# Optimization experiments

Measured on AMD Instinct MI355X. Metric: run time of the kernel, lower is better.

Reference implementation:

```python
import jax, jax.numpy as jnp
import numpy as np


def _rotate_half(x):
    x1, x2 = jnp.split(x, 2, axis=-1)
    return jnp.concatenate([-x2, x1], axis=-1)


def _rope_tables(seq_len, head_dim, base=10000.0):
    inv_freq = 1.0 / (base ** (jnp.arange(0, head_dim, 2, dtype=jnp.float32) / head_dim))
    t = jnp.arange(seq_len, dtype=jnp.float32)
    freqs = jnp.outer(t, inv_freq)  # [S, head_dim/2]
    # torch .repeat(...,2) tiles along last dim -> concat
    cos = jnp.concatenate([jnp.cos(freqs), jnp.cos(freqs)], axis=-1)  # [S, head_dim]
    sin = jnp.concatenate([jnp.sin(freqs), jnp.sin(freqs)], axis=-1)
    return cos[None, None], sin[None, None]  # [1,1,S,head_dim]


def setup_inputs() -> dict:
    key = jax.random.key(0)
    ks = jax.random.split(key, 5)
    B, S, D = 2, 2048, 2048
    sd = 1.0 / np.sqrt(D)
    return {
        "x": jax.random.normal(ks[0], (B, S, D), dtype=jnp.float32),
        "Wq": jax.random.normal(ks[1], (D, D), dtype=jnp.float32) * sd,
        "Wk": jax.random.normal(ks[2], (D, D), dtype=jnp.float32) * sd,
        "Wv": jax.random.normal(ks[3], (D, D), dtype=jnp.float32) * sd,
        "Wo": jax.random.normal(ks[4], (D, D), dtype=jnp.float32) * sd,
        "n_heads": 16,
    }


def reference(x, Wq, Wk, Wv, Wo, n_heads):
    B, S, D = x.shape
    hd = D // n_heads
    # projections (torch Linear: x @ W.T)
    def proj(W):
        return (x @ W.T).reshape(B, S, n_heads, hd).transpose(0, 2, 1, 3)  # [B,H,S,hd]
    q, k, v = proj(Wq), proj(Wk), proj(Wv)
    cos, sin = _rope_tables(S, hd)
    q = q * cos + _rotate_half(q) * sin
    k = k * cos + _rotate_half(k) * sin
    scale = 1.0 / np.sqrt(hd)
    scores = jnp.einsum('bhsd,bhtd->bhst', q, k) * scale  # [B,H,S,S]
    causal = jnp.triu(jnp.ones((S, S), dtype=bool), k=1)
    scores = jnp.where(causal[None, None], -jnp.inf, scores)
    attn = jax.nn.softmax(scores, axis=-1)
    out = jnp.einsum('bhst,bhtd->bhsd', attn, v)
    out = out.transpose(0, 2, 1, 3).reshape(B, S, D)
    return out @ Wo.T
```

## Files before the change

kernel.cpp:

```cpp
#include <hip/hip_runtime.h>
#include <hip/hip_bf16.h>
#include <math.h>

typedef __attribute__((ext_vector_type(8))) short bf16x8;
typedef __attribute__((ext_vector_type(4))) float f32x4;

#define GLB_CAST(p) ((const __attribute__((address_space(1))) void*)(p))
#define LDS_CAST(p) ((__attribute__((address_space(3))) void*)(p))

static __device__ __forceinline__ unsigned short bf16_bits(float x) {
    __hip_bfloat16 h = __float2bfloat16(x);
    return *(unsigned short*)&h;
}

__global__ void cvt_f32_bf16(const float* __restrict__ s, __hip_bfloat16* __restrict__ d, int n) {
    int i = (blockIdx.x * 256 + threadIdx.x) * 8;
    if (i >= n) return;
    float4 a = *(const float4*)(s + i);
    float4 b = *(const float4*)(s + i + 4);
    float t[8] = {a.x, a.y, a.z, a.w, b.x, b.y, b.z, b.w};
    union { unsigned short u[8]; uint4 v; } o;
#pragma unroll
    for (int j = 0; j < 8; ++j) o.u[j] = bf16_bits(t[j]);
    *(uint4*)(d + i) = o.v;
}

template <int EPI>
__global__ __launch_bounds__(256, 2)
void gemm_bt(const __hip_bfloat16* __restrict__ A,
             const __hip_bfloat16* __restrict__ Bt,
             void* __restrict__ Cout)
{
    const int K = 2048;
    __shared__ __hip_bfloat16 As[128 * 32];
    __shared__ __hip_bfloat16 Bs[128 * 32];
    const int tid = threadIdx.x;
    const int w = tid >> 6, l = tid & 63;
    const int m0 = blockIdx.x * 128, n0 = blockIdx.y * 128;
    const int wr = w >> 1, wc = w & 1;
    const int lr = l & 15, kh = l >> 4;

    f32x4 acc[4][4] = {};

    for (int kt = 0; kt < 64; ++kt) {
        const int kb = kt * 32;
#pragma unroll
        for (int i = 0; i < 2; ++i) {
            const int s = i * 256 + tid;
            const int r = s >> 2, ks = (s & 3) * 8;
            __builtin_amdgcn_global_load_lds(GLB_CAST(A + (size_t)(m0 + r) * K + kb + ks),
                                             LDS_CAST(As + (size_t)(i * 256 + w * 64) * 8),
                                             16, 0, 0);
            __builtin_amdgcn_global_load_lds(GLB_CAST(Bt + (size_t)(n0 + r) * K + kb + ks),
                                             LDS_CAST(Bs + (size_t)(i * 256 + w * 64) * 8),
                                             16, 0, 0);
        }
        __syncthreads();
        bf16x8 af[4], bfr[4];
#pragma unroll
        for (int m = 0; m < 4; ++m)
            af[m] = *(const bf16x8*)(As + (wr * 64 + m * 16 + lr) * 32 + kh * 8);
#pragma unroll
        for (int n = 0; n < 4; ++n)
            bfr[n] = *(const bf16x8*)(Bs + (wc * 64 + n * 16 + lr) * 32 + kh * 8);
#pragma unroll
        for (int m = 0; m < 4; ++m)
#pragma unroll
            for (int n = 0; n < 4; ++n)
                acc[m][n] = __builtin_amdgcn_mfma_f32_16x16x32_bf16(af[m], bfr[n], acc[m][n], 0, 0, 0);
        __syncthreads();
    }

#pragma unroll
    for (int m = 0; m < 4; ++m) {
        const int r0 = m0 + wr * 64 + m * 16 + kh * 4;
#pragma unroll
        for (int n = 0; n < 4; ++n) {
            const int c = n0 + wc * 64 + n * 16 + lr;
#pragma unroll
            for (int j = 0; j < 4; ++j) {
                const int r = r0 + j;
                const float v = acc[m][n][j];
                if (EPI == 0) {
                    const int b = r >> 11, sy = r & 2047, h = c >> 7, dd = c & 127;
                    ((__hip_bfloat16*)Cout)[((size_t)(b * 16 + h) * 2048 + sy) * 128 + dd] =
                        __float2bfloat16(v);
                } else if (EPI == 2) {
                    const int b = r >> 11, sy = r & 2047, h = c >> 7, dd = c & 127;
                    ((__hip_bfloat16*)Cout)[((size_t)(b * 16 + h) * 128 + dd) * 2048 + sy] =
                        __float2bfloat16(v);
                } else {
                    ((float*)Cout)[(size_t)r * 2048 + c] = v;
                }
            }
        }
    }
}

__global__ void rope_qk(__hip_bfloat16* __restrict__ Q, __hip_bfloat16* __restrict__ Kk) {
    const int row = blockIdx.x * 4 + (threadIdx.x >> 6);
    const int j = threadIdx.x & 63;
    const int s = row & 2047;
    const float inv = __expf((float)j * (-0.14391156831212787f));
    float sn, c;
    __sincosf((float)s * inv, &sn, &c);
    const size_t base = (size_t)row * 128;
    float q1 = __bfloat162float(Q[base + j]);
    float q2 = __bfloat162float(Q[base + 64 + j]);
    Q[base + j]      = __float2bfloat16(q1 * c - q2 * sn);
    Q[base + 64 + j] = __float2bfloat16(q2 * c + q1 * sn);
    float k1 = __bfloat162float(Kk[base + j]);
    float k2 = __bfloat162float(Kk[base + 64 + j]);
    Kk[base + j]      = __float2bfloat16(k1 * c - k2 * sn);
    Kk[base + 64 + j] = __float2bfloat16(k2 * c + k1 * sn);
}

__global__ __launch_bounds__(256, 4)
void flash_part(const __hip_bfloat16* __restrict__ Q,
                const __hip_bfloat16* __restrict__ K,
                const __hip_bfloat16* __restrict__ Vt,
                __hip_bfloat16* __restrict__ AO,
                __hip_bfloat16* __restrict__ OP,
                float* __restrict__ ML)
{
    const int bh = blockIdx.x;
    const int u  = blockIdx.y;
    const int tid = threadIdx.x, w = tid >> 6, l = tid & 63;
    const int lr = l & 15, hi = l >> 4;

    int G, part, P;
    if (u < 32)      { G = 24 + (u >> 2);            part = u & 3;       P = 4; }
    else if (u < 56) { int v = u - 32; G = 16 + v/3; part = v % 3;       P = 3; }
    else if (u < 72) { int v = u - 56; G = 8 + (v>>1); part = v & 1;     P = 2; }
    else             { G = u - 72;                   part = 0;           P = 1; }
    const int nt = 2 * G + 2;
    const int t0 = (part * nt) / P, t1 = ((part + 1) * nt) / P;
    const bool split = (P > 1);
    const int qb = G * 64 + w * 16;
    const int q_own = qb + lr;

    const __hip_bfloat16* Qb = Q  + (size_t)bh * 2048 * 128;
    const __hip_bfloat16* Kb = K  + (size_t)bh * 2048 * 128;
    const __hip_bfloat16* Vb = Vt + (size_t)bh * 128 * 2048;

    __shared__ __align__(16) __hip_bfloat16 Ks[2][32 * 128];
    __shared__ __align__(16) __hip_bfloat16 Vs[2][128 * 32];

    bf16x8 qf[4];
#pragma unroll
    for (int kk = 0; kk < 4; ++kk)
        qf[kk] = *(const bf16x8*)(Qb + (size_t)(qb + lr) * 128 + kk * 32 + hi * 8);

    int rK[2], cK[2], rV[2], cV[2];
#pragma unroll
    for (int i = 0; i < 2; ++i) {
        const int ci = i * 4 + w;
        rK[i] = ci * 4 + (l >> 4);
        cK[i] = ((l & 15) ^ (rK[i] & 7)) * 8;
        rV[i] = ci * 16 + (l >> 2);
        cV[i] = ((l & 3) ^ (rV[i] & 3)) * 8;
    }
    const int rsw7 = lr & 7, vsw3 = lr & 3;
    const int sA = lr + ((hi & 1) << 5);
    const int sB = sA + 16;
    const bool plo = (hi < 2);

#define STAGE(buf, t)                                                                        \
    {                                                                                        \
        const int kv0_ = (t) * 32;                                                           \
        _Pragma("unroll")                                                                    \
        for (int i = 0; i < 2; ++i) {                                                        \
            __builtin_amdgcn_global_load_lds(                                                \
                GLB_CAST(Kb + (size_t)(kv0_ + rK[i]) * 128 + cK[i]),                         \
                LDS_CAST(&Ks[buf][(i * 4 + w) * 512]), 16, 0, 0);                            \
            __builtin_amdgcn_global_load_lds(                                                \
                GLB_CAST(Vb + (size_t)rV[i] * 2048 + kv0_ + cV[i]),                          \
                LDS_CAST(&Vs[buf][(i * 4 + w) * 512]), 16, 0, 0);                            \
        }                                                                                    \
    }

    f32x4 o[8] = {};
    float mrow = -1e30f, lrow = 0.f;
    const float scale = 0.08838834764831845f;

    int cur = 0;
    STAGE(0, t0);
    __syncthreads();

    for (int t = t0; t < t1; ++t) {
        if (t + 1 < t1) STAGE(cur ^ 1, t + 1);
        const __hip_bfloat16* Kc = &Ks[cur][0];
        const __hip_bfloat16* Vc = &Vs[cur][0];
        const int kv0 = t * 32;

        f32x4 sT[2] = {};
#pragma unroll
        for (int f = 0; f < 2; ++f)
#pragma unroll
            for (int kk = 0; kk < 4; ++kk) {
                const bf16x8 kf = *(const bf16x8*)(Kc + (f * 16 + lr) * 128 +
                                                   ((kk * 4 + hi) ^ rsw7) * 8);
                sT[f] = __builtin_amdgcn_mfma_f32_16x16x32_bf16(kf, qf[kk], sT[f], 0, 0, 0);
            }

        float val[8];
        float pmax = -1e30f;
#pragma unroll
        for (int f = 0; f < 2; ++f)
#pragma unroll
            for (int j = 0; j < 4; ++j) {
                const int kv = kv0 + f * 16 + hi * 4 + j;
                float v = sT[f][j] * scale;
                v = (kv > q_own) ? -1e30f : v;
                val[f * 4 + j] = v;
                pmax = fmaxf(pmax, v);
            }
        pmax = fmaxf(pmax, __shfl_xor(pmax, 16));
        pmax = fmaxf(pmax, __shfl_xor(pmax, 32));

        if (!__all(pmax <= mrow + 8.f)) {
            const float mnew = fmaxf(mrow, pmax);
            const float alpha = __expf(mrow - mnew);
            mrow = mnew;
            lrow *= alpha;
            float aj[4];
#pragma unroll
            for (int j = 0; j < 4; ++j)
                aj[j] = __shfl(alpha, (l & 48) | (hi * 4 + j), 64);
#pragma unroll
            for (int dn = 0; dn < 8; ++dn)
#pragma unroll
                for (int j = 0; j < 4; ++j) o[dn][j] *= aj[j];
        }

        float p[8];
        float rs = 0.f;
#pragma unroll
        for (int i = 0; i < 8; ++i) { p[i] = __expf(val[i] - mrow); rs += p[i]; }
        rs += __shfl_xor(rs, 16);
        rs += __shfl_xor(rs, 32);
        lrow += rs;

        unsigned wds[4];
#pragma unroll
        for (int i = 0; i < 4; ++i)
            wds[i] = (unsigned)bf16_bits(p[i * 2]) | ((unsigned)bf16_bits(p[i * 2 + 1]) << 16);

        const unsigned a0 = __shfl((int)wds[0], sA, 64), a1 = __shfl((int)wds[1], sA, 64);
        const unsigned a2 = __shfl((int)wds[2], sA, 64), a3 = __shfl((int)wds[3], sA, 64);
        const unsigned b0 = __shfl((int)wds[0], sB, 64), b1 = __shfl((int)wds[1], sB, 64);
        const unsigned b2 = __shfl((int)wds[2], sB, 64), b3 = __shfl((int)wds[3], sB, 64);
        union { unsigned u[4]; bf16x8 v; } pf;
        pf.u[0] = plo ? a0 : a2;
        pf.u[1] = plo ? a1 : a3;
        pf.u[2] = plo ? b0 : b2;
        pf.u[3] = plo ? b1 : b3;

#pragma unroll
        for (int dn = 0; dn < 8; ++dn) {
            const bf16x8 vf = *(const bf16x8*)(Vc + (dn * 16 + lr) * 32 + (hi ^ vsw3) * 8);
            o[dn] = __builtin_amdgcn_mfma_f32_16x16x32_bf16(pf.v, vf, o[dn], 0, 0, 0);
        }
        __syncthreads();
        cur ^= 1;
    }
#undef STAGE

    if (!split) {
        float linv[4];
#pragma unroll
        for (int j = 0; j < 4; ++j)
            linv[j] = 1.0f / __shfl(lrow, (l & 48) | (hi * 4 + j), 64);
#pragma unroll
        for (int j = 0; j < 4; ++j) {
            const int q = qb + hi * 4 + j;
            const size_t rb = ((size_t)(bh >> 4) * 2048 + q) * 2048 + (size_t)(bh & 15) * 128;
#pragma unroll
            for (int dn = 0; dn < 8; ++dn)
                AO[rb + dn * 16 + lr] = __float2bfloat16(o[dn][j] * linv[j]);
        }
    } else {
        const int base = (G < 16) ? (G - 8) * 2 : ((G < 24) ? 16 + (G - 16) * 3
                                                            : 40 + (G - 24) * 4);
        const int pidx = bh * 72 + base + part;
#pragma unroll
        for (int j = 0; j < 4; ++j) {
            const int row = w * 16 + hi * 4 + j;
#pragma unroll
            for (int dn = 0; dn < 8; ++dn)
                OP[((size_t)pidx * 64 + row) * 128 + dn * 16 + lr] = __float2bfloat16(o[dn][j]);
        }
        if (l < 16) {
            ML[((size_t)pidx * 64 + w * 16 + l) * 2]     = mrow;
            ML[((size_t)pidx * 64 + w * 16 + l) * 2 + 1] = lrow;
        }
    }
}

__global__ void flash_merge(const __hip_bfloat16* __restrict__ OP,
                            const float* __restrict__ ML,
                            __hip_bfloat16* __restrict__ AO)
{
    const int gi = blockIdx.x % 24, bh = blockIdx.x / 24;
    const int G = 8 + gi;
    const int P = (G < 16) ? 2 : ((G < 24) ? 3 : 4);
    const int base = (G < 16) ? (G - 8) * 2 : ((G < 24) ? 16 + (G - 16) * 3
                                                        : 40 + (G - 24) * 4);
    const int pidx0 = bh * 72 + base;
    const int t = threadIdx.x, r = t >> 2, c0 = (t & 3) * 32;

    float m[4], lv[4];
    float M = -1e30f;
#pragma unroll
    for (int p = 0; p < 4; ++p) if (p < P) {
        m[p]  = ML[((size_t)(pidx0 + p) * 64 + r) * 2];
        lv[p] = ML[((size_t)(pidx0 + p) * 64 + r) * 2 + 1];
        M = fmaxf(M, m[p]);
    }
    float wgt[4];
    float den = 0.f;
#pragma unroll
    for (int p = 0; p < 4; ++p) if (p < P) {
        wgt[p] = __expf(m[p] - M);
        den += lv[p] * wgt[p];
    }
    const float inv = 1.0f / den;

    const int q = G * 64 + r;
    __hip_bfloat16* out = AO + ((size_t)(bh >> 4) * 2048 + q) * 2048 + (size_t)(bh & 15) * 128 + c0;

#pragma unroll
    for (int ch = 0; ch < 4; ++ch) {
        float acc[8] = {0.f, 0.f, 0.f, 0.f, 0.f, 0.f, 0.f, 0.f};
#pragma unroll
        for (int p = 0; p < 4; ++p) if (p < P) {
            const bf16x8 v = *(const bf16x8*)(OP + ((size_t)(pidx0 + p) * 64 + r) * 128 + c0 + ch * 8);
#pragma unroll
            for (int i = 0; i < 8; ++i) {
                __hip_bfloat16 hv;
                *(short*)&hv = v[i];
                acc[i] += __bfloat162float(hv) * wgt[p];
            }
        }
        union { unsigned short us[8]; bf16x8 v; } rr;
#pragma unroll
        for (int i = 0; i < 8; ++i) rr.us[i] = bf16_bits(acc[i] * inv);
        *(bf16x8*)(out + ch * 8) = rr.v;
    }
}

extern "C" void kernel_launch(void* const* d_in, const int* in_sizes, int n_in,
                              void* d_out, int out_size, void* d_ws, size_t ws_size,
                              hipStream_t stream) {
    (void)in_sizes; (void)n_in; (void)out_size; (void)ws_size;
    const float* x  = (const float*)d_in[0];
    const float* Wq = (const float*)d_in[1];
    const float* Wk = (const float*)d_in[2];
    const float* Wv = (const float*)d_in[3];
    const float* Wo = (const float*)d_in[4];

    char* p = (char*)d_ws;
    auto carve = [&](size_t bytes) -> char* {
        char* r = p;
        p += (bytes + 255) & ~(size_t)255;
        return r;
    };
    __hip_bfloat16* xb  = (__hip_bfloat16*)carve(4096ull * 2048 * 2);
    __hip_bfloat16* Wqb = (__hip_bfloat16*)carve(2048ull * 2048 * 2);
    __hip_bfloat16* Wkb = (__hip_bfloat16*)carve(2048ull * 2048 * 2);
    __hip_bfloat16* Wvb = (__hip_bfloat16*)carve(2048ull * 2048 * 2);
    __hip_bfloat16* Wob = (__hip_bfloat16*)carve(2048ull * 2048 * 2);
    __hip_bfloat16* Qb  = (__hip_bfloat16*)carve(32ull * 2048 * 128 * 2);
    __hip_bfloat16* Kb  = (__hip_bfloat16*)carve(32ull * 2048 * 128 * 2);
    __hip_bfloat16* Vtb = (__hip_bfloat16*)carve(32ull * 128 * 2048 * 2);
    __hip_bfloat16* OPb = (__hip_bfloat16*)carve(32ull * 72 * 64 * 128 * 2);
    float*          MLb = (float*)carve(32ull * 72 * 64 * 2 * 4);

    cvt_f32_bf16<<<4096, 256, 0, stream>>>(x,  xb,  4096 * 2048);
    cvt_f32_bf16<<<2048, 256, 0, stream>>>(Wq, Wqb, 2048 * 2048);
    cvt_f32_bf16<<<2048, 256, 0, stream>>>(Wk, Wkb, 2048 * 2048);
    cvt_f32_bf16<<<2048, 256, 0, stream>>>(Wv, Wvb, 2048 * 2048);
    cvt_f32_bf16<<<2048, 256, 0, stream>>>(Wo, Wob, 2048 * 2048);

    dim3 gg(32, 16);
    gemm_bt<0><<<gg, 256, 0, stream>>>(xb, Wqb, Qb);
    gemm_bt<0><<<gg, 256, 0, stream>>>(xb, Wkb, Kb);
    gemm_bt<2><<<gg, 256, 0, stream>>>(xb, Wvb, Vtb);

    rope_qk<<<16384, 256, 0, stream>>>(Qb, Kb);

    flash_part<<<dim3(32, 80), 256, 0, stream>>>(Qb, Kb, Vtb, xb , OPb, MLb);
    flash_merge<<<768, 256, 0, stream>>>(OPb, MLb, xb );

    gemm_bt<1><<<gg, 256, 0, stream>>>(xb, Wob, (float*)d_out);
}
```

Baseline: 322.5 us.

## Enlarge flash query tile to 128, merge QKV GEMMs and conversion kernels

Each flash_part wave now processes two 16-row query groups, so every K/V tile staged in LDS feeds twice as many MFMAs and the grid halves. The split-KV partition table and merge kernel are rescaled to match, and occupancy is lowered to 3 blocks per SM to make room for the larger register state. Separately, the five f32-to-bf16 conversions are fused into one launch and the Q/K/V projection GEMMs run as a single grid-stacked launch, cutting launch overhead and tail effects. The doubled accumulators raise register pressure and may cost occupancy.

```diff
diff --git a/kernel.cpp b/kernel.cpp
--- a/kernel.cpp
+++ b/kernel.cpp
@@ -13,23 +13,109 @@
     return *(unsigned short*)&h;
 }
 
-__global__ void cvt_f32_bf16(const float* __restrict__ s, __hip_bfloat16* __restrict__ d, int n) {
-    int i = (blockIdx.x * 256 + threadIdx.x) * 8;
-    if (i >= n) return;
-    float4 a = *(const float4*)(s + i);
-    float4 b = *(const float4*)(s + i + 4);
+__global__ void cvt_all(const float* __restrict__ x,  const float* __restrict__ wq,
+                        const float* __restrict__ wk, const float* __restrict__ wv,
+                        const float* __restrict__ wo,
+                        __hip_bfloat16* __restrict__ xb,  __hip_bfloat16* __restrict__ wqb,
+                        __hip_bfloat16* __restrict__ wkb, __hip_bfloat16* __restrict__ wvb,
+                        __hip_bfloat16* __restrict__ wob)
+{
+    const size_t NX = 8388608, NW = 4194304;
+    size_t i = ((size_t)blockIdx.x * 256 + threadIdx.x) * 8;
+    const float* s; __hip_bfloat16* d; size_t off;
+    if (i < NX) { s = x; d = xb; off = i; }
+    else {
+        size_t k = i - NX;
+        const int seg = (int)(k >> 22);
+        off = k & (NW - 1);
+        s = seg == 0 ? wq : seg == 1 ? wk : seg == 2 ? wv : wo;
+        d = seg == 0 ? wqb : seg == 1 ? wkb : seg == 2 ? wvb : wob;
+    }
+    float4 a = *(const float4*)(s + off);
+    float4 b = *(const float4*)(s + off + 4);
     float t[8] = {a.x, a.y, a.z, a.w, b.x, b.y, b.z, b.w};
     union { unsigned short u[8]; uint4 v; } o;
 #pragma unroll
     for (int j = 0; j < 8; ++j) o.u[j] = bf16_bits(t[j]);
-    *(uint4*)(d + i) = o.v;
-}
-
-template <int EPI>
+    *(uint4*)(d + off) = o.v;
+}
+
 __global__ __launch_bounds__(256, 2)
-void gemm_bt(const __hip_bfloat16* __restrict__ A,
-             const __hip_bfloat16* __restrict__ Bt,
-             void* __restrict__ Cout)
+void gemm_qkv(const __hip_bfloat16* __restrict__ A,
+              const __hip_bfloat16* __restrict__ Wq,
+              const __hip_bfloat16* __restrict__ Wk,
+              const __hip_bfloat16* __restrict__ Wv,
+              __hip_bfloat16* __restrict__ Qo,
+              __hip_bfloat16* __restrict__ Ko,
+              __hip_bfloat16* __restrict__ Vto)
+{
+    const int K = 2048;
+    __shared__ __hip_bfloat16 As[128 * 32];
+    __shared__ __hip_bfloat16 Bs[128 * 32];
+    const int tid = threadIdx.x;
+    const int w = tid >> 6, l = tid & 63;
+    const int sel = blockIdx.y >> 4;
+    const __hip_bfloat16* Bt = sel == 0 ? Wq : (sel == 1 ? Wk : Wv);
+    const int m0 = blockIdx.x * 128, n0 = (blockIdx.y & 15) * 128;
+    const int wr = w >> 1, wc = w & 1;
+    const int lr = l & 15, kh = l >> 4;
+
+    f32x4 acc[4][4] = {};
+
+    for (int kt = 0; kt < 64; ++kt) {
+        const int kb = kt * 32;
+#pragma unroll
+        for (int i = 0; i < 2; ++i) {
+            const int s = i * 256 + tid;
+            const int r = s >> 2, ks = (s & 3) * 8;
+            __builtin_amdgcn_global_load_lds(GLB_CAST(A + (size_t)(m0 + r) * K + kb + ks),
+                                             LDS_CAST(As + (size_t)(i * 256 + w * 64) * 8),
+                                             16, 0, 0);
+            __builtin_amdgcn_global_load_lds(GLB_CAST(Bt + (size_t)(n0 + r) * K + kb + ks),
+                                             LDS_CAST(Bs + (size_t)(i * 256 + w * 64) * 8),
+                                             16, 0, 0);
+        }
+        __syncthreads();
+        bf16x8 af[4], bfr[4];
+#pragma unroll
+        for (int m = 0; m < 4; ++m)
+            af[m] = *(const bf16x8*)(As + (wr * 64 + m * 16 + lr) * 32 + kh * 8);
+#pragma unroll
+        for (int n = 0; n < 4; ++n)
+            bfr[n] = *(const bf16x8*)(Bs + (wc * 64 + n * 16 + lr) * 32 + kh * 8);
+#pragma unroll
+        for (int m = 0; m < 4; ++m)
+#pragma unroll
+            for (int n = 0; n < 4; ++n)
+                acc[m][n] = __builtin_amdgcn_mfma_f32_16x16x32_bf16(af[m], bfr[n], acc[m][n], 0, 0, 0);
+        __syncthreads();
+    }
+
+    __hip_bfloat16* Cout = sel == 0 ? Qo : (sel == 1 ? Ko : Vto);
+#pragma unroll
+    for (int m = 0; m < 4; ++m) {
+        const int r0 = m0 + wr * 64 + m * 16 + kh * 4;
+#pragma unroll
+        for (int n = 0; n < 4; ++n) {
+            const int c = n0 + wc * 64 + n * 16 + lr;
+#pragma unroll
+            for (int j = 0; j < 4; ++j) {
+                const int r = r0 + j;
+                const float v = acc[m][n][j];
+                const int b = r >> 11, sy = r & 2047, h = c >> 7, dd = c & 127;
+                if (sel < 2)
+                    Cout[((size_t)(b * 16 + h) * 2048 + sy) * 128 + dd] = __float2bfloat16(v);
+                else
+                    Cout[((size_t)(b * 16 + h) * 128 + dd) * 2048 + sy] = __float2bfloat16(v);
+            }
+        }
+    }
+}
+
+__global__ __launch_bounds__(256, 2)
+void gemm_o(const __hip_bfloat16* __restrict__ A,
+            const __hip_bfloat16* __restrict__ Bt,
+            float* __restrict__ Cout)
 {
     const int K = 2048;
     __shared__ __hip_bfloat16 As[128 * 32];
@@ -78,21 +164,8 @@
         for (int n = 0; n < 4; ++n) {
             const int c = n0 + wc * 64 + n * 16 + lr;
 #pragma unroll
-            for (int j = 0; j < 4; ++j) {
-                const int r = r0 + j;
-                const float v = acc[m][n][j];
-                if (EPI == 0) {
-                    const int b = r >> 11, sy = r & 2047, h = c >> 7, dd = c & 127;
-                    ((__hip_bfloat16*)Cout)[((size_t)(b * 16 + h) * 2048 + sy) * 128 + dd] =
-                        __float2bfloat16(v);
-                } else if (EPI == 2) {
-                    const int b = r >> 11, sy = r & 2047, h = c >> 7, dd = c & 127;
-                    ((__hip_bfloat16*)Cout)[((size_t)(b * 16 + h) * 128 + dd) * 2048 + sy] =
-                        __float2bfloat16(v);
-                } else {
-                    ((float*)Cout)[(size_t)r * 2048 + c] = v;
-                }
-            }
+            for (int j = 0; j < 4; ++j)
+                Cout[(size_t)(r0 + j) * 2048 + c] = acc[m][n][j];
         }
     }
 }
@@ -115,7 +188,7 @@
     Kk[base + 64 + j] = __float2bfloat16(k2 * c + k1 * sn);
 }
 
-__global__ __launch_bounds__(256, 4)
+__global__ __launch_bounds__(256, 3)
 void flash_part(const __hip_bfloat16* __restrict__ Q,
                 const __hip_bfloat16* __restrict__ K,
                 const __hip_bfloat16* __restrict__ Vt,
@@ -129,15 +202,15 @@
     const int lr = l & 15, hi = l >> 4;
 
     int G, part, P;
-    if (u < 32)      { G = 24 + (u >> 2);            part = u & 3;       P = 4; }
-    else if (u < 56) { int v = u - 32; G = 16 + v/3; part = v % 3;       P = 3; }
-    else if (u < 72) { int v = u - 56; G = 8 + (v>>1); part = v & 1;     P = 2; }
-    else             { G = u - 72;                   part = 0;           P = 1; }
-    const int nt = 2 * G + 2;
+    if (u < 16)      { G = 12 + (u >> 2);            part = u & 3;   P = 4; }
+    else if (u < 28) { int v = u - 16; G = 8 + v / 3; part = v % 3;  P = 3; }
+    else if (u < 36) { int v = u - 28; G = 4 + (v >> 1); part = v & 1; P = 2; }
+    else             { G = u - 36;                   part = 0;       P = 1; }
+    const int nt = 4 * G + 4;
     const int t0 = (part * nt) / P, t1 = ((part + 1) * nt) / P;
     const bool split = (P > 1);
-    const int qb = G * 64 + w * 16;
-    const int q_own = qb + lr;
+    const int qb = G * 128 + w * 32;
+    const int q0 = qb + lr, q1 = qb + 16 + lr;
 
     const __hip_bfloat16* Qb = Q  + (size_t)bh * 2048 * 128;
     const __hip_bfloat16* Kb = K  + (size_t)bh * 2048 * 128;
@@ -146,10 +219,12 @@
     __shared__ __align__(16) __hip_bfloat16 Ks[2][32 * 128];
     __shared__ __align__(16) __hip_bfloat16 Vs[2][128 * 32];
 
-    bf16x8 qf[4];
-#pragma unroll
-    for (int kk = 0; kk < 4; ++kk)
-        qf[kk] = *(const bf16x8*)(Qb + (size_t)(qb + lr) * 128 + kk * 32 + hi * 8);
+    bf16x8 qf[2][4];
+#pragma unroll
+    for (int g = 0; g < 2; ++g)
+#pragma unroll
+        for (int kk = 0; kk < 4; ++kk)
+            qf[g][kk] = *(const bf16x8*)(Qb + (size_t)(qb + g * 16 + lr) * 128 + kk * 32 + hi * 8);
 
     int rK[2], cK[2], rV[2], cV[2];
 #pragma unroll
@@ -179,8 +254,9 @@
         }                                                                                    \
     }
 
-    f32x4 o[8] = {};
-    float mrow = -1e30f, lrow = 0.f;
+    f32x4 o[2][8] = {};
+    float mrow[2] = {-1e30f, -1e30f};
+    float lrow[2] = {0.f, 0.f};
     const float scale = 0.08838834764831845f;
 
     int cur = 0;
@@ -193,73 +269,92 @@
         const __hip_bfloat16* Vc = &Vs[cur][0];
         const int kv0 = t * 32;
 
-        f32x4 sT[2] = {};
+        f32x4 sT[2][2] = {};
 #pragma unroll
         for (int f = 0; f < 2; ++f)
 #pragma unroll
             for (int kk = 0; kk < 4; ++kk) {
                 const bf16x8 kf = *(const bf16x8*)(Kc + (f * 16 + lr) * 128 +
                                                    ((kk * 4 + hi) ^ rsw7) * 8);
-                sT[f] = __builtin_amdgcn_mfma_f32_16x16x32_bf16(kf, qf[kk], sT[f], 0, 0, 0);
-            }
-
-        float val[8];
-        float pmax = -1e30f;
-#pragma unroll
-        for (int f = 0; f < 2; ++f)
-#pragma unroll
-            for (int j = 0; j < 4; ++j) {
-                const int kv = kv0 + f * 16 + hi * 4 + j;
-                float v = sT[f][j] * scale;
-                v = (kv > q_own) ? -1e30f : v;
-                val[f * 4 + j] = v;
-                pmax = fmaxf(pmax, v);
-            }
-        pmax = fmaxf(pmax, __shfl_xor(pmax, 16));
-        pmax = fmaxf(pmax, __shfl_xor(pmax, 32));
-
-        if (!__all(pmax <= mrow + 8.f)) {
-            const float mnew = fmaxf(mrow, pmax);
-            const float alpha = __expf(mrow - mnew);
-            mrow = mnew;
-            lrow *= alpha;
-            float aj[4];
-#pragma unroll
-            for (int j = 0; j < 4; ++j)
-                aj[j] = __shfl(alpha, (l & 48) | (hi * 4 + j), 64);
-#pragma unroll
-            for (int dn = 0; dn < 8; ++dn)
-#pragma unroll
-                for (int j = 0; j < 4; ++j) o[dn][j] *= aj[j];
-        }
-
-        float p[8];
-        float rs = 0.f;
-#pragma unroll
-        for (int i = 0; i < 8; ++i) { p[i] = __expf(val[i] - mrow); rs += p[i]; }
-        rs += __shfl_xor(rs, 16);
-        rs += __shfl_xor(rs, 32);
-        lrow += rs;
-
-        unsigned wds[4];
-#pragma unroll
-        for (int i = 0; i < 4; ++i)
-            wds[i] = (unsigned)bf16_bits(p[i * 2]) | ((unsigned)bf16_bits(p[i * 2 + 1]) << 16);
-
-        const unsigned a0 = __shfl((int)wds[0], sA, 64), a1 = __shfl((int)wds[1], sA, 64);
-        const unsigned a2 = __shfl((int)wds[2], sA, 64), a3 = __shfl((int)wds[3], sA, 64);
-        const unsigned b0 = __shfl((int)wds[0], sB, 64), b1 = __shfl((int)wds[1], sB, 64);
-        const unsigned b2 = __shfl((int)wds[2], sB, 64), b3 = __shfl((int)wds[3], sB, 64);
-        union { unsigned u[4]; bf16x8 v; } pf;
-        pf.u[0] = plo ? a0 : a2;
-        pf.u[1] = plo ? a1 : a3;
-        pf.u[2] = plo ? b0 : b2;
-        pf.u[3] = plo ? b1 : b3;
+                sT[0][f] = __builtin_amdgcn_mfma_f32_16x16x32_bf16(kf, qf[0][kk], sT[0][f], 0, 0, 0);
+                sT[1][f] = __builtin_amdgcn_mfma_f32_16x16x32_bf16(kf, qf[1][kk], sT[1][f], 0, 0, 0);
+            }
+
+        float pmax[2] = {-1e30f, -1e30f};
+#pragma unroll
+        for (int g = 0; g < 2; ++g) {
+            const int qown = g ? q1 : q0;
+#pragma unroll
+            for (int f = 0; f < 2; ++f)
+#pragma unroll
+                for (int j = 0; j < 4; ++j) {
+                    const int kv = kv0 + f * 16 + hi * 4 + j;
+                    float v = sT[g][f][j] * scale;
+                    v = (kv > qown) ? -1e30f : v;
+                    sT[g][f][j] = v;
+                    pmax[g] = fmaxf(pmax[g], v);
+                }
+            pmax[g] = fmaxf(pmax[g], __shfl_xor(pmax[g], 16));
+            pmax[g] = fmaxf(pmax[g], __shfl_xor(pmax[g], 32));
+        }
+
+        if (!__all(pmax[0] <= mrow[0] + 8.f && pmax[1] <= mrow[1] + 8.f)) {
+#pragma unroll
+            for (int g = 0; g < 2; ++g) {
+                const float mnew = fmaxf(mrow[g], pmax[g]);
+                const float alpha = __expf(mrow[g] - mnew);
+                mrow[g] = mnew;
+                lrow[g] *= alpha;
+                float aj[4];
+#pragma unroll
+                for (int j = 0; j < 4; ++j)
+                    aj[j] = __shfl(alpha, (l & 48) | (hi * 4 + j), 64);
+#pragma unroll
+                for (int dn = 0; dn < 8; ++dn)
+#pragma unroll
+                    for (int j = 0; j < 4; ++j) o[g][dn][j] *= aj[j];
+            }
+        }
+
+#pragma unroll
+        for (int g = 0; g < 2; ++g) {
+            float rs = 0.f;
+#pragma unroll
+            for (int f = 0; f < 2; ++f)
+#pragma unroll
+                for (int j = 0; j < 4; ++j) {
+                    const float pv = __expf(sT[g][f][j] - mrow[g]);
+                    sT[g][f][j] = pv;
+                    rs += pv;
+                }
+            rs += __shfl_xor(rs, 16);
+            rs += __shfl_xor(rs, 32);
+            lrow[g] += rs;
+        }
+
+        union { unsigned u[4]; bf16x8 v; } pf[2];
+#pragma unroll
+        for (int g = 0; g < 2; ++g) {
+            unsigned wds[4];
+#pragma unroll
+            for (int i = 0; i < 4; ++i)
+                wds[i] = (unsigned)bf16_bits(sT[g][i >> 1][(i & 1) * 2]) |
+                         ((unsigned)bf16_bits(sT[g][i >> 1][(i & 1) * 2 + 1]) << 16);
+            const unsigned a0 = __shfl((int)wds[0], sA, 64), a1 = __shfl((int)wds[1], sA, 64);
+            const unsigned a2 = __shfl((int)wds[2], sA, 64), a3 = __shfl((int)wds[3], sA, 64);
+            const unsigned b0 = __shfl((int)wds[0], sB, 64), b1 = __shfl((int)wds[1], sB, 64);
+            const unsigned b2 = __shfl((int)wds[2], sB, 64), b3 = __shfl((int)wds[3], sB, 64);
+            pf[g].u[0] = plo ? a0 : a2;
+            pf[g].u[1] = plo ? a1 : a3;
+            pf[g].u[2] = plo ? b0 : b2;
+            pf[g].u[3] = plo ? b1 : b3;
+        }
 
 #pragma unroll
         for (int dn = 0; dn < 8; ++dn) {
             const bf16x8 vf = *(const bf16x8*)(Vc + (dn * 16 + lr) * 32 + (hi ^ vsw3) * 8);
-            o[dn] = __builtin_amdgcn_mfma_f32_16x16x32_bf16(pf.v, vf, o[dn], 0, 0, 0);
+            o[0][dn] = __builtin_amdgcn_mfma_f32_16x16x32_bf16(pf[0].v, vf, o[0][dn], 0, 0, 0);
+            o[1][dn] = __builtin_amdgcn_mfma_f32_16x16x32_bf16(pf[1].v, vf, o[1][dn], 0, 0, 0);
         }
         __syncthreads();
         cur ^= 1;
@@ -267,32 +362,40 @@
 #undef STAGE
 
     if (!split) {
-        float linv[4];
-#pragma unroll
-        for (int j = 0; j < 4; ++j)
-            linv[j] = 1.0f / __shfl(lrow, (l & 48) | (hi * 4 + j), 64);
-#pragma unroll
-        for (int j = 0; j < 4; ++j) {
-            const int q = qb + hi * 4 + j;
-            const size_t rb = ((size_t)(bh >> 4) * 2048 + q) * 2048 + (size_t)(bh & 15) * 128;
-#pragma unroll
-            for (int dn = 0; dn < 8; ++dn)
-                AO[rb + dn * 16 + lr] = __float2bfloat16(o[dn][j] * linv[j]);
+#pragma unroll
+        for (int g = 0; g < 2; ++g) {
+            float linv[4];
+#pragma unroll
+            for (int j = 0; j < 4; ++j)
+                linv[j] = 1.0f / __shfl(lrow[g], (l & 48) | (hi * 4 + j), 64);
+#pragma unroll
+            for (int j = 0; j < 4; ++j) {
+                const int q = qb + g * 16 + hi * 4 + j;
+                const size_t rb = ((size_t)(bh >> 4) * 2048 + q) * 2048 + (size_t)(bh & 15) * 128;
+#pragma unroll
+                for (int dn = 0; dn < 8; ++dn)
+                    AO[rb + dn * 16 + lr] = __float2bfloat16(o[g][dn][j] * linv[j]);
+            }
         }
     } else {
-        const int base = (G < 16) ? (G - 8) * 2 : ((G < 24) ? 16 + (G - 16) * 3
-                                                            : 40 + (G - 24) * 4);
-        const int pidx = bh * 72 + base + part;
-#pragma unroll
-        for (int j = 0; j < 4; ++j) {
-            const int row = w * 16 + hi * 4 + j;
-#pragma unroll
-            for (int dn = 0; dn < 8; ++dn)
-                OP[((size_t)pidx * 64 + row) * 128 + dn * 16 + lr] = __float2bfloat16(o[dn][j]);
-        }
-        if (l < 16) {
-            ML[((size_t)pidx * 64 + w * 16 + l) * 2]     = mrow;
-            ML[((size_t)pidx * 64 + w * 16 + l) * 2 + 1] = lrow;
+        const int base = (G < 8) ? (G - 4) * 2 : ((G < 12) ? 8 + (G - 8) * 3
+                                                           : 20 + (G - 12) * 4);
+        const int pidx = bh * 36 + base + part;
+#pragma unroll
+        for (int g = 0; g < 2; ++g) {
+#pragma unroll
+            for (int j = 0; j < 4; ++j) {
+                const int row = w * 32 + g * 16 + hi * 4 + j;
+#pragma unroll
+                for (int dn = 0; dn < 8; ++dn)
+                    OP[((size_t)pidx * 128 + row) * 128 + dn * 16 + lr] =
+                        __float2bfloat16(o[g][dn][j]);
+            }
+            if (l < 16) {
+                const int row = w * 32 + g * 16 + l;
+                ML[((size_t)pidx * 128 + row) * 2]     = mrow[g];
+                ML[((size_t)pidx * 128 + row) * 2 + 1] = lrow[g];
+            }
         }
     }
 }
@@ -301,20 +404,20 @@
                             const float* __restrict__ ML,
                             __hip_bfloat16* __restrict__ AO)
 {
-    const int gi = blockIdx.x % 24, bh = blockIdx.x / 24;
-    const int G = 8 + gi;
-    const int P = (G < 16) ? 2 : ((G < 24) ? 3 : 4);
-    const int base = (G < 16) ? (G - 8) * 2 : ((G < 24) ? 16 + (G - 16) * 3
-                                                        : 40 + (G - 24) * 4);
-    const int pidx0 = bh * 72 + base;
-    const int t = threadIdx.x, r = t >> 2, c0 = (t & 3) * 32;
+    const int gi = blockIdx.x % 12, bh = blockIdx.x / 12;
+    const int G = 4 + gi;
+    const int P = (G < 8) ? 2 : ((G < 12) ? 3 : 4);
+    const int base = (G < 8) ? (G - 4) * 2 : ((G < 12) ? 8 + (G - 8) * 3
+                                                       : 20 + (G - 12) * 4);
+    const int pidx0 = bh * 36 + base;
+    const int t = threadIdx.x, r = t >> 1, c0 = (t & 1) * 64;
 
     float m[4], lv[4];
     float M = -1e30f;
 #pragma unroll
     for (int p = 0; p < 4; ++p) if (p < P) {
-        m[p]  = ML[((size_t)(pidx0 + p) * 64 + r) * 2];
-        lv[p] = ML[((size_t)(pidx0 + p) * 64 + r) * 2 + 1];
+        m[p]  = ML[((size_t)(pidx0 + p) * 128 + r) * 2];
+        lv[p] = ML[((size_t)(pidx0 + p) * 128 + r) * 2 + 1];
         M = fmaxf(M, m[p]);
     }
     float wgt[4];
@@ -326,15 +429,15 @@
     }
     const float inv = 1.0f / den;
 
-    const int q = G * 64 + r;
+    const int q = G * 128 + r;
     __hip_bfloat16* out = AO + ((size_t)(bh >> 4) * 2048 + q) * 2048 + (size_t)(bh & 15) * 128 + c0;
 
 #pragma unroll
-    for (int ch = 0; ch < 4; ++ch) {
+    for (int ch = 0; ch < 8; ++ch) {
         float acc[8] = {0.f, 0.f, 0.f, 0.f, 0.f, 0.f, 0.f, 0.f};
 #pragma unroll
         for (int p = 0; p < 4; ++p) if (p < P) {
-            const bf16x8 v = *(const bf16x8*)(OP + ((size_t)(pidx0 + p) * 64 + r) * 128 + c0 + ch * 8);
+            const bf16x8 v = *(const bf16x8*)(OP + ((size_t)(pidx0 + p) * 128 + r) * 128 + c0 + ch * 8);
 #pragma unroll
             for (int i = 0; i < 8; ++i) {
                 __hip_bfloat16 hv;
@@ -373,24 +476,17 @@
     __hip_bfloat16* Qb  = (__hip_bfloat16*)carve(32ull * 2048 * 128 * 2);
     __hip_bfloat16* Kb  = (__hip_bfloat16*)carve(32ull * 2048 * 128 * 2);
     __hip_bfloat16* Vtb = (__hip_bfloat16*)carve(32ull * 128 * 2048 * 2);
-    __hip_bfloat16* OPb = (__hip_bfloat16*)carve(32ull * 72 * 64 * 128 * 2);
-    float*          MLb = (float*)carve(32ull * 72 * 64 * 2 * 4);
-
-    cvt_f32_bf16<<<4096, 256, 0, stream>>>(x,  xb,  4096 * 2048);
-    cvt_f32_bf16<<<2048, 256, 0, stream>>>(Wq, Wqb, 2048 * 2048);
-    cvt_f32_bf16<<<2048, 256, 0, stream>>>(Wk, Wkb, 2048 * 2048);
-    cvt_f32_bf16<<<2048, 256, 0, stream>>>(Wv, Wvb, 2048 * 2048);
-    cvt_f32_bf16<<<2048, 256, 0, stream>>>(Wo, Wob, 2048 * 2048);
-
-    dim3 gg(32, 16);
-    gemm_bt<0><<<gg, 256, 0, stream>>>(xb, Wqb, Qb);
-    gemm_bt<0><<<gg, 256, 0, stream>>>(xb, Wkb, Kb);
-    gemm_bt<2><<<gg, 256, 0, stream>>>(xb, Wvb, Vtb);
+    __hip_bfloat16* OPb = (__hip_bfloat16*)carve(32ull * 36 * 128 * 128 * 2);
+    float*          MLb = (float*)carve(32ull * 36 * 128 * 2 * 4);
+
+    cvt_all<<<12288, 256, 0, stream>>>(x, Wq, Wk, Wv, Wo, xb, Wqb, Wkb, Wvb, Wob);
+
+    gemm_qkv<<<dim3(32, 48), 256, 0, stream>>>(xb, Wqb, Wkb, Wvb, Qb, Kb, Vtb);
 
     rope_qk<<<16384, 256, 0, stream>>>(Qb, Kb);
 
-    flash_part<<<dim3(32, 80), 256, 0, stream>>>(Qb, Kb, Vtb, xb , OPb, MLb);
-    flash_merge<<<768, 256, 0, stream>>>(OPb, MLb, xb );
-
-    gemm_bt<1><<<gg, 256, 0, stream>>>(xb, Wob, (float*)d_out);
-}
+    flash_part<<<dim3(32, 40), 256, 0, stream>>>(Qb, Kb, Vtb, xb , OPb, MLb);
+    flash_merge<<<384, 256, 0, stream>>>(OPb, MLb, xb );
+
+    gemm_o<<<dim3(32, 16), 256, 0, stream>>>(xb, Wob, (float*)d_out);
+}
```

Result: no change. 323.1 us (+0.2%).
